# Kernel tuning notes

Hardware: AMD Instinct MI355X
Metric: run time of the kernel (lower is better)

The kernel has to match this reference:

```python
import jax, jax.numpy as jnp
import numpy as np

N_DENSE = 13
N_SPARSE = 26
VOCAB = 10000
N_FIELD = N_DENSE + N_SPARSE  # 39
N_FEAT = N_DENSE + N_SPARSE * VOCAB  # 260013
K = 8
BATCH = 4096
# offset of each sparse feature's one-hot block inside the flattened feature axis
OFFSETS = jnp.asarray(N_DENSE + np.arange(N_SPARSE) * VOCAB, dtype=jnp.int32)  # (26,)


def setup_inputs() -> dict:
    key = jax.random.key(0)
    k1, k2, k3, k4 = jax.random.split(key, 4)
    dense_x = jax.random.normal(k1, (BATCH, N_DENSE), dtype=jnp.float32)
    sparse_x = jax.random.randint(k2, (BATCH, N_SPARSE), 0, VOCAB, dtype=jnp.int32)
    w0 = jnp.zeros((1,), dtype=jnp.float32)
    w = jax.random.normal(k3, (N_FEAT, 1), dtype=jnp.float32) * 0.05
    v = jax.random.normal(k4, (N_FEAT, N_FIELD, K), dtype=jnp.float32) * 0.05
    return {"dense_x": dense_x, "sparse_x": sparse_x, "w0": w0, "w": w, "v": v}


def reference(dense_x, sparse_x, w0, w, v):
    # Mathematically identical to one_hot(sparse) concat dense then dense GEMMs:
    # one-hot @ table == row gather; dense part keeps its continuous values.
    idx = OFFSETS[None, :] + sparse_x  # (B, 26) global feature indices

    # linear term: x @ w + w0
    linear = dense_x @ w[:N_DENSE] + jnp.sum(w[idx, 0], axis=1, keepdims=True) + w0  # (B,1)

    # field_f = tensordot(x, v, axes=1)  -> (B, n_field, k)
    field_f = jnp.einsum('bd,dfk->bfk', dense_x, v[:N_DENSE]) + jnp.sum(v[idx], axis=1)

    # sum_{i<j} <f_i, f_j> = 0.5 * ((sum_i f_i)^2 - sum_i f_i^2) summed over k
    s = jnp.sum(field_f, axis=1)  # (B, K)
    cross = 0.5 * (jnp.sum(s * s, axis=1) - jnp.sum(field_f * field_f, axis=(1, 2)))  # (B,)

    return jax.nn.sigmoid(linear + cross[:, None])  # (B, 1)
```

## Files before the change

kernel.cpp:

```cpp
#include <hip/hip_runtime.h>
#include <math.h>

#define BATCH    4096
#define ND       13
#define NS       26
#define VOCAB    10000
#define NFIELD   39
#define KDIM     8
#define ROW      (NFIELD * KDIM)
#define NT       320
#define NWAVE    5

__global__ __launch_bounds__(NT) void ffm_kernel(
    const float* __restrict__ dense_x,
    const int*   __restrict__ sparse_x,
    const float* __restrict__ w0,
    const float* __restrict__ w,
    const float* __restrict__ v,
    float*       __restrict__ out)
{
    const int b = blockIdx.x;
    const int t = threadIdx.x;

    __shared__ int   s_idx[NS];
    __shared__ float s_dense[ND];
    __shared__ float s_part[NWAVE * KDIM];
    __shared__ float sq_part[NWAVE];

    if (t < NS) {
        s_idx[t] = ND + t * VOCAB + sparse_x[b * NS + t];
    }
    if (t >= 64 && t < 64 + ND) {
        s_dense[t - 64] = dense_x[b * ND + (t - 64)];
    }
    __syncthreads();

    float acc = 0.f;
    if (t < ROW) {
#pragma unroll
        for (int d = 0; d < ND; ++d)
            acc = fmaf(s_dense[d], v[d * ROW + t], acc);
#pragma unroll
        for (int j = 0; j < NS; ++j)
            acc += v[(size_t)s_idx[j] * ROW + t];
    }

    float sq = acc * acc;
#pragma unroll
    for (int m = 32; m >= 1; m >>= 1)
        sq += __shfl_xor(sq, m, 64);

    float sk = acc;
    sk += __shfl_xor(sk, 8, 64);
    sk += __shfl_xor(sk, 16, 64);
    sk += __shfl_xor(sk, 32, 64);

    const int wave = t >> 6;
    const int lane = t & 63;
    if (lane < KDIM) s_part[wave * KDIM + lane] = sk;
    if (lane == 0)   sq_part[wave] = sq;
    __syncthreads();

    if (t < 64) {
        float contrib = 0.f;
        if (t < KDIM) {
            float s = 0.f;
#pragma unroll
            for (int wv = 0; wv < NWAVE; ++wv) s += s_part[wv * KDIM + t];
            contrib += 0.5f * s * s;
        }
        if (t < NS)
            contrib += w[s_idx[t]];
        if (t >= 32 && t < 32 + ND)
            contrib += s_dense[t - 32] * w[t - 32];
        if (t == 63) {
            float ss = 0.f;
#pragma unroll
            for (int wv = 0; wv < NWAVE; ++wv) ss += sq_part[wv];
            contrib += w0[0] - 0.5f * ss;
        }
#pragma unroll
        for (int m = 32; m >= 1; m >>= 1)
            contrib += __shfl_xor(contrib, m, 64);
        if (t == 0)
            out[b] = 1.f / (1.f + expf(-contrib));
    }
}

extern "C" void kernel_launch(void* const* d_in, const int* in_sizes, int n_in,
                              void* d_out, int out_size, void* d_ws, size_t ws_size,
                              hipStream_t stream) {
    const float* dense_x  = (const float*)d_in[0];
    const int*   sparse_x = (const int*)d_in[1];
    const float* w0       = (const float*)d_in[2];
    const float* w        = (const float*)d_in[3];
    const float* v        = (const float*)d_in[4];
    float* out = (float*)d_out;

    hipLaunchKernelGGL(ffm_kernel, dim3(BATCH), dim3(NT), 0, stream,
                       dense_x, sparse_x, w0, w, v, out);
}
```

Baseline: 28.62 us.

## Vectorize row gathers as float4 and pack two batch rows per block

Each thread now loads float4 slices of the embedding rows (78 slots per 312-float row) instead of scalar floats, which cuts the number of load instructions. Each 256-thread block handles two batch rows, with a half-block of two waves per row. The linear term is computed in a separate wave path that runs alongside the gather. The k-dimension reduction is adapted to the float4 layout by splitting even and odd lanes, and readfirstlane makes the row index uniform so addressing can use scalar registers. The trade-offs are fewer idle threads per row but more lanes left unused (78 of 128) and fewer blocks in flight.

```diff
diff --git a/kernel.cpp b/kernel.cpp
--- a/kernel.cpp
+++ b/kernel.cpp
@@ -7,9 +7,12 @@
 #define VOCAB    10000
 #define NFIELD   39
 #define KDIM     8
-#define ROW      (NFIELD * KDIM)
-#define NT       320
-#define NWAVE    5
+#define ROW      312
+#define NSLOT    78
+#define RPB      2
+#define NT       256
+
+typedef float f4 __attribute__((ext_vector_type(4)));
 
 __global__ __launch_bounds__(NT) void ffm_kernel(
     const float* __restrict__ dense_x,
@@ -19,71 +22,74 @@
     const float* __restrict__ v,
     float*       __restrict__ out)
 {
-    const int b = blockIdx.x;
-    const int t = threadIdx.x;
+    const int t    = threadIdx.x;
+    const int h    = t >> 7;
+    const int lt   = t & 127;
+    const int b    = blockIdx.x * RPB + h;
+    const int wv   = t >> 6;
+    const int lane = t & 63;
 
-    __shared__ int   s_idx[NS];
-    __shared__ float s_dense[ND];
-    __shared__ float s_part[NWAVE * KDIM];
-    __shared__ float sq_part[NWAVE];
+    __shared__ int   s_idx[RPB][NS];
+    __shared__ float s_dense[RPB][ND];
+    __shared__ f4    s_sA[4];
+    __shared__ f4    s_sB[4];
+    __shared__ float s_sq[4];
+    __shared__ float s_lin[RPB];
 
-    if (t < NS) {
-        s_idx[t] = ND + t * VOCAB + sparse_x[b * NS + t];
-    }
-    if (t >= 64 && t < 64 + ND) {
-        s_dense[t - 64] = dense_x[b * ND + (t - 64)];
-    }
+    if (lt < NS)
+        s_idx[h][lt] = ND + lt * VOCAB + sparse_x[b * NS + lt];
+    if (lt >= 32 && lt < 32 + ND)
+        s_dense[h][lt - 32] = dense_x[b * ND + (lt - 32)];
     __syncthreads();
 
-    float acc = 0.f;
-    if (t < ROW) {
+    if ((lt >> 6) == 0) {
+        float li = 0.f;
+        if (lane < NS)                li = w[s_idx[h][lane]];
+        else if (lane < NS + ND)      li = s_dense[h][lane - NS] * w[lane - NS];
+        else if (lane == NS + ND)     li = w0[0];
+#pragma unroll
+        for (int m = 32; m >= 1; m >>= 1) li += __shfl_xor(li, m, 64);
+        if (lane == 0) s_lin[h] = li;
+    }
+
+    f4 acc = 0.f;
+    if (lt < NSLOT) {
+        const f4* vp = (const f4*)v;
 #pragma unroll
         for (int d = 0; d < ND; ++d)
-            acc = fmaf(s_dense[d], v[d * ROW + t], acc);
+            acc += s_dense[h][d] * vp[d * NSLOT + lt];
 #pragma unroll
-        for (int j = 0; j < NS; ++j)
-            acc += v[(size_t)s_idx[j] * ROW + t];
+        for (int j = 0; j < NS; ++j) {
+            int idx = __builtin_amdgcn_readfirstlane(s_idx[h][j]);
+            const f4* rowp = (const f4*)(v + (size_t)idx * ROW);
+            acc += rowp[lt];
+        }
     }
 
-    float sq = acc * acc;
+    float sq = acc[0]*acc[0] + acc[1]*acc[1] + acc[2]*acc[2] + acc[3]*acc[3];
 #pragma unroll
-    for (int m = 32; m >= 1; m >>= 1)
-        sq += __shfl_xor(sq, m, 64);
+    for (int m = 32; m >= 1; m >>= 1) sq += __shfl_xor(sq, m, 64);
 
-    float sk = acc;
-    sk += __shfl_xor(sk, 8, 64);
-    sk += __shfl_xor(sk, 16, 64);
-    sk += __shfl_xor(sk, 32, 64);
-
-    const int wave = t >> 6;
-    const int lane = t & 63;
-    if (lane < KDIM) s_part[wave * KDIM + lane] = sk;
-    if (lane == 0)   sq_part[wave] = sq;
+    f4 sv = acc;
+#pragma unroll
+    for (int m = 32; m >= 2; m >>= 1) {
+        sv[0] += __shfl_xor(sv[0], m, 64);
+        sv[1] += __shfl_xor(sv[1], m, 64);
+        sv[2] += __shfl_xor(sv[2], m, 64);
+        sv[3] += __shfl_xor(sv[3], m, 64);
+    }
+    if (lane == 0) { s_sA[wv] = sv; s_sq[wv] = sq; }
+    if (lane == 1) { s_sB[wv] = sv; }
     __syncthreads();
 
-    if (t < 64) {
-        float contrib = 0.f;
-        if (t < KDIM) {
-            float s = 0.f;
-#pragma unroll
-            for (int wv = 0; wv < NWAVE; ++wv) s += s_part[wv * KDIM + t];
-            contrib += 0.5f * s * s;
-        }
-        if (t < NS)
-            contrib += w[s_idx[t]];
-        if (t >= 32 && t < 32 + ND)
-            contrib += s_dense[t - 32] * w[t - 32];
-        if (t == 63) {
-            float ss = 0.f;
-#pragma unroll
-            for (int wv = 0; wv < NWAVE; ++wv) ss += sq_part[wv];
-            contrib += w0[0] - 0.5f * ss;
-        }
-#pragma unroll
-        for (int m = 32; m >= 1; m >>= 1)
-            contrib += __shfl_xor(contrib, m, 64);
-        if (t == 0)
-            out[b] = 1.f / (1.f + expf(-contrib));
+    if (lt == 0) {
+        f4 A = s_sA[2*h] + s_sA[2*h + 1];
+        f4 B = s_sB[2*h] + s_sB[2*h + 1];
+        float ssum  = A[0]*A[0] + A[1]*A[1] + A[2]*A[2] + A[3]*A[3]
+                    + B[0]*B[0] + B[1]*B[1] + B[2]*B[2] + B[3]*B[3];
+        float sumsq = s_sq[2*h] + s_sq[2*h + 1];
+        float total = s_lin[h] + 0.5f * (ssum - sumsq);
+        out[b] = 1.f / (1.f + expf(-total));
     }
 }
 
@@ -97,6 +103,6 @@
     const float* v        = (const float*)d_in[4];
     float* out = (float*)d_out;
 
-    hipLaunchKernelGGL(ffm_kernel, dim3(BATCH), dim3(NT), 0, stream,
+    hipLaunchKernelGGL(ffm_kernel, dim3(BATCH / RPB), dim3(NT), 0, stream,
                        dense_x, sparse_x, w0, w, v, out);
 }
```

Result: slower. 29.25 us (+2.2%).
